# Performance work log

Hardware: AMD Instinct MI355X
Metric: run time of the kernel (lower is better)

The kernel has to match this reference:

```python
import jax, jax.numpy as jnp
import numpy as np

# model hyperparameters (from init_kwargs)
N_IN = 2048
NN = 512
BATCH = 64
DT, TAU_M, TAU_X = 0.05, 10.0, 2.0
ALPHA = 1.0 - DT / TAU_M   # membrane decay
BETA = 1.0 - DT / TAU_X    # lateral-trace decay
V_TH = 2.0


def _loo_idx(nn):
    # leave-one-out gather indices: idx[j, n] = j if j < n else j + 1
    j = np.arange(nn - 1)[:, None]
    n = np.arange(nn)[None, :]
    return jnp.asarray(j + (j >= n))  # (nn-1, nn) int


def setup_inputs() -> dict:
    key = jax.random.key(0)
    k1, k2, k3, k4 = jax.random.split(key, 4)
    x = jax.random.uniform(k1, (BATCH, N_IN, NN), dtype=jnp.float32)      # per-neuron external input
    v = jax.random.normal(k2, (BATCH, NN), dtype=jnp.float32)             # membrane state
    z = jnp.zeros((BATCH, NN), dtype=jnp.float32)                         # previous spikes
    z_out = jax.random.uniform(k3, (BATCH, NN), dtype=jnp.float32)        # lateral spike trace
    w = jax.random.normal(k4, (N_IN + NN - 1, NN), dtype=jnp.float32) / np.sqrt(N_IN)
    return {"x": x, "v": v, "z": z, "z_out": z_out, "w": w}


def reference(x, v, z, z_out, w):
    # update lateral trace: z_out = beta * z_out + z (z detached in original)
    z_out_new = BETA * z_out + z
    # leave-one-out lateral input: z_loo[b, j, n] = z_out_new[b, j + (j >= n)]
    idx = _loo_idx(NN)
    z_loo = z_out_new[:, idx]  # (B, NN-1, NN)
    # membrane drive: sum_k x_tot[b,k,n] * w[k,n], where x_tot = cat([x, z_loo], dim=1)
    drive = (jnp.einsum('bkn,kn->bn', x, w[:N_IN])
             + jnp.einsum('bjn,jn->bn', z_loo, w[N_IN:]))
    v_new = ALPHA * v + drive - V_TH * z
    # thresholding nonlinearity -> output spikes
    z_new = (v_new - V_TH > 0).astype(v.dtype)
    return v_new, z_new, z_out_new
```

## Files before the change

kernel.cpp:

```cpp
#include <hip/hip_runtime.h>

#define BATCH 64
#define N_IN  2048
#define NN    512
#define NCH   64
#define THREADS 1024
#define ALPHA 0.995f
#define BETA  0.975f
#define V_TH  2.0f

__global__ __launch_bounds__(THREADS)
void fused_step(const float* __restrict__ x,
                const float* __restrict__ v,
                const float* __restrict__ z,
                const float* __restrict__ z_out,
                const float* __restrict__ w,
                float* __restrict__ out)
{
    const int b   = blockIdx.y;
    const int nb  = blockIdx.x * NCH;
    const int tid = threadIdx.x;
    const int nl  = tid & 15;
    const int kk  = tid >> 4;

    __shared__ float  zlds[NN];
    __shared__ float4 red[THREADS];
    __shared__ float  red2[THREADS];

    for (int i = tid; i < NN; i += THREADS) {
        zlds[i] = BETA * z_out[b * NN + i] + z[b * NN + i];
    }

    const float4* __restrict__ x4 = (const float4*)(x + (size_t)b * N_IN * NN + nb);
    const float4* __restrict__ w4 = (const float4*)(w + nb);
    float4 acc = make_float4(0.f, 0.f, 0.f, 0.f);
#pragma unroll 8
    for (int k = kk; k < N_IN; k += 64) {
        const float4 xv = x4[(size_t)k * (NN / 4) + nl];
        const float4 wv = w4[(size_t)k * (NN / 4) + nl];
        acc.x += xv.x * wv.x;
        acc.y += xv.y * wv.y;
        acc.z += xv.z * wv.z;
        acc.w += xv.w * wv.w;
    }
    red[tid] = acc;
    __syncthreads();
#pragma unroll
    for (int s = 512; s >= 16; s >>= 1) {
        if (tid < s) {
            const float4 o = red[tid + s];
            red[tid].x += o.x; red[tid].y += o.y;
            red[tid].z += o.z; red[tid].w += o.w;
        }
        __syncthreads();
    }

    const int n_loc = tid & 63;
    const int n     = nb + n_loc;
    const int jg    = tid >> 6;
    float d2 = 0.f;
    for (int j = jg; j < NN - 1; j += 16) {
        d2 += zlds[j + (j >= n)] * w[(size_t)(N_IN + j) * NN + n];
    }
    red2[tid] = d2;
    __syncthreads();

    if (tid < 64) {
        const float d1 = ((const float*)red)[n_loc];
        float d2s = 0.f;
#pragma unroll
        for (int g = 0; g < 16; ++g) d2s += red2[n_loc + 64 * g];
        const float vv = v[b * NN + n];
        const float zz = z[b * NN + n];
        const float v_new = ALPHA * vv + d1 + d2s - V_TH * zz;
        out[b * NN + n]                  = v_new;
        out[BATCH * NN + b * NN + n]     = (v_new - V_TH > 0.f) ? 1.f : 0.f;
        out[2 * BATCH * NN + b * NN + n] = zlds[n];
    }
}

extern "C" void kernel_launch(void* const* d_in, const int* in_sizes, int n_in,
                              void* d_out, int out_size, void* d_ws, size_t ws_size,
                              hipStream_t stream) {
    (void)in_sizes; (void)n_in; (void)out_size; (void)d_ws; (void)ws_size;
    const float* x     = (const float*)d_in[0];
    const float* v     = (const float*)d_in[1];
    const float* z     = (const float*)d_in[2];
    const float* z_out = (const float*)d_in[3];
    const float* w     = (const float*)d_in[4];
    float* out = (float*)d_out;

    dim3 grid(NN / NCH, BATCH);
    fused_step<<<grid, THREADS, 0, stream>>>(x, v, z, z_out, w, out);
}
```

Measured before the change: 62.12 us.

## Split into K-split drive kernel and finish kernel with coalesced full-row loads

Splits the fused kernel in two. The first kernel splits the input dimension into 8 chunks per batch, reads full 512-wide rows with float4 loads and unrolls four loads at a time, then writes per-chunk partial sums to the workspace. The second kernel, one block per batch, sums the partials, computes the lateral leave-one-out term for all 512 neurons and writes the outputs. This is meant to improve load coalescing and memory-level parallelism and to shorten the long shared-memory reduction tree, at the cost of an extra launch and a workspace round-trip.

```diff
diff --git a/kernel.cpp b/kernel.cpp
--- a/kernel.cpp
+++ b/kernel.cpp
@@ -3,75 +3,96 @@
 #define BATCH 64
 #define N_IN  2048
 #define NN    512
-#define NCH   64
-#define THREADS 1024
+#define KR    8
 #define ALPHA 0.995f
 #define BETA  0.975f
 #define V_TH  2.0f
 
-__global__ __launch_bounds__(THREADS)
-void fused_step(const float* __restrict__ x,
-                const float* __restrict__ v,
-                const float* __restrict__ z,
-                const float* __restrict__ z_out,
-                const float* __restrict__ w,
-                float* __restrict__ out)
+__global__ __launch_bounds__(1024, 8)
+void k1_drive1(const float* __restrict__ x,
+               const float* __restrict__ w,
+               float* __restrict__ ws)
 {
+    const int kr  = blockIdx.x;
     const int b   = blockIdx.y;
-    const int nb  = blockIdx.x * NCH;
     const int tid = threadIdx.x;
-    const int nl  = tid & 15;
-    const int kk  = tid >> 4;
+    const int c4  = tid & 127;
+    const int kl  = tid >> 7;
 
-    __shared__ float  zlds[NN];
-    __shared__ float4 red[THREADS];
-    __shared__ float  red2[THREADS];
+    const float4* __restrict__ x4 = (const float4*)x;
+    const float4* __restrict__ w4 = (const float4*)w;
 
-    for (int i = tid; i < NN; i += THREADS) {
-        zlds[i] = BETA * z_out[b * NN + i] + z[b * NN + i];
+    const float4* xp = x4 + ((size_t)b * N_IN + kr * 256 + kl) * 128 + c4;
+    const float4* wp = w4 + ((size_t)(kr * 256 + kl)) * 128 + c4;
+    const size_t  ks = 8 * 128;
+
+    float4 acc = make_float4(0.f, 0.f, 0.f, 0.f);
+#pragma unroll
+    for (int i = 0; i < 8; ++i) {
+        float4 xv[4], wv[4];
+#pragma unroll
+        for (int u = 0; u < 4; ++u) xv[u] = xp[u * ks];
+#pragma unroll
+        for (int u = 0; u < 4; ++u) wv[u] = wp[u * ks];
+#pragma unroll
+        for (int u = 0; u < 4; ++u) {
+            acc.x += xv[u].x * wv[u].x;
+            acc.y += xv[u].y * wv[u].y;
+            acc.z += xv[u].z * wv[u].z;
+            acc.w += xv[u].w * wv[u].w;
+        }
+        xp += 4 * ks;
+        wp += 4 * ks;
     }
 
-    const float4* __restrict__ x4 = (const float4*)(x + (size_t)b * N_IN * NN + nb);
-    const float4* __restrict__ w4 = (const float4*)(w + nb);
-    float4 acc = make_float4(0.f, 0.f, 0.f, 0.f);
-#pragma unroll 8
-    for (int k = kk; k < N_IN; k += 64) {
-        const float4 xv = x4[(size_t)k * (NN / 4) + nl];
-        const float4 wv = w4[(size_t)k * (NN / 4) + nl];
-        acc.x += xv.x * wv.x;
-        acc.y += xv.y * wv.y;
-        acc.z += xv.z * wv.z;
-        acc.w += xv.w * wv.w;
-    }
+    __shared__ float4 red[1024];
     red[tid] = acc;
     __syncthreads();
+    if (tid < 128) {
+        float4 s = red[tid];
 #pragma unroll
-    for (int s = 512; s >= 16; s >>= 1) {
-        if (tid < s) {
-            const float4 o = red[tid + s];
-            red[tid].x += o.x; red[tid].y += o.y;
-            red[tid].z += o.z; red[tid].w += o.w;
+        for (int g = 1; g < 8; ++g) {
+            const float4 o = red[tid + 128 * g];
+            s.x += o.x; s.y += o.y; s.z += o.z; s.w += o.w;
         }
-        __syncthreads();
+        ((float4*)ws)[((size_t)kr * BATCH + b) * 128 + tid] = s;
     }
+}
 
-    const int n_loc = tid & 63;
-    const int n     = nb + n_loc;
-    const int jg    = tid >> 6;
-    float d2 = 0.f;
-    for (int j = jg; j < NN - 1; j += 16) {
-        d2 += zlds[j + (j >= n)] * w[(size_t)(N_IN + j) * NN + n];
-    }
-    red2[tid] = d2;
+__global__ __launch_bounds__(1024)
+void k2_finish(const float* __restrict__ v,
+               const float* __restrict__ z,
+               const float* __restrict__ z_out,
+               const float* __restrict__ w,
+               const float* __restrict__ ws,
+               float* __restrict__ out)
+{
+    const int b   = blockIdx.x;
+    const int tid = threadIdx.x;
+    const int n   = tid & 511;
+    const int jh  = tid >> 9;
+
+    __shared__ float zlds[NN];
+    __shared__ float r2[1024];
+
+    if (tid < NN)
+        zlds[tid] = BETA * z_out[b * NN + tid] + z[b * NN + tid];
     __syncthreads();
 
-    if (tid < 64) {
-        const float d1 = ((const float*)red)[n_loc];
-        float d2s = 0.f;
+    float d2 = 0.f;
+    for (int j = jh; j < NN - 1; j += 2)
+        d2 += zlds[j + (j >= n)] * w[(size_t)(N_IN + j) * NN + n];
+    r2[tid] = d2;
+    __syncthreads();
+
+    if (tid < NN) {
+        float d1 = 0.f;
 #pragma unroll
-        for (int g = 0; g < 16; ++g) d2s += red2[n_loc + 64 * g];
-        const float vv = v[b * NN + n];
-        const float zz = z[b * NN + n];
+        for (int kr = 0; kr < KR; ++kr)
+            d1 += ws[((size_t)kr * BATCH + b) * NN + n];
+        const float d2s   = r2[n] + r2[n + 512];
+        const float vv    = v[b * NN + n];
+        const float zz    = z[b * NN + n];
         const float v_new = ALPHA * vv + d1 + d2s - V_TH * zz;
         out[b * NN + n]                  = v_new;
         out[BATCH * NN + b * NN + n]     = (v_new - V_TH > 0.f) ? 1.f : 0.f;
@@ -82,14 +103,16 @@
 extern "C" void kernel_launch(void* const* d_in, const int* in_sizes, int n_in,
                               void* d_out, int out_size, void* d_ws, size_t ws_size,
                               hipStream_t stream) {
-    (void)in_sizes; (void)n_in; (void)out_size; (void)d_ws; (void)ws_size;
+    (void)in_sizes; (void)n_in; (void)out_size; (void)ws_size;
     const float* x     = (const float*)d_in[0];
     const float* v     = (const float*)d_in[1];
     const float* z     = (const float*)d_in[2];
     const float* z_out = (const float*)d_in[3];
     const float* w     = (const float*)d_in[4];
     float* out = (float*)d_out;
+    float* ws  = (float*)d_ws;
 
-    dim3 grid(NN / NCH, BATCH);
-    fused_step<<<grid, THREADS, 0, stream>>>(x, v, z, z_out, w, out);
+    dim3 g1(KR, BATCH);
+    k1_drive1<<<g1, 1024, 0, stream>>>(x, w, ws);
+    k2_finish<<<BATCH, 1024, 0, stream>>>(v, z, z_out, w, ws, out);
 }
```

Result: slower. 113.2 us (+82.2%).
